# Performance work log

Measured on AMD Instinct MI355X. Metric: run time of the kernel, lower is better.

Reference implementation:

```python
import jax, jax.numpy as jnp
import numpy as np
from jax.scipy.special import logsumexp

TAU = 0.05
ITERATIONS = 10


def setup_inputs() -> dict:
    key = jax.random.key(0)
    logits = jax.random.normal(key, (256, 512, 512), dtype=jnp.float32)
    return {"logits": logits}


def reference(logits) -> jnp.ndarray:
    # log-space Sinkhorn-Knopp: project logits/tau to a doubly stochastic matrix
    Z = logits / TAU  # [B, n, n]
    u0 = jnp.zeros(Z.shape[:-1], dtype=Z.dtype)  # [B, n] row potentials
    v0 = jnp.zeros_like(u0)                      # [B, n] col potentials
    # log_marginal is zeros(n) in the original, i.e. uniform target marginals of 1

    def body(_, uv):
        u, v = uv
        u = -logsumexp(Z + v[..., None, :], axis=-1)  # row normalization
        v = -logsumexp(Z + u[..., :, None], axis=-2)  # col normalization
        return (u, v)

    u, v = jax.lax.fori_loop(0, ITERATIONS, body, (u0, v0))
    return jnp.exp(Z + u[..., :, None] + v[..., None, :])
```

## Files before the change

kernel.cpp:

```cpp
#include <hip/hip_runtime.h>

#define BN 512
#define NW 16
#define RPW 32

static constexpr float kScale = 28.853900817779268f;

__device__ __forceinline__ float fexp2(float x){ return __builtin_amdgcn_exp2f(x); }
__device__ __forceinline__ float flog2(float x){ return __builtin_amdgcn_logf(x); }
__device__ __forceinline__ float frcp (float x){ return __builtin_amdgcn_rcpf(x); }

__device__ __forceinline__ float dpp_sum64(float s){
    int t;
    t = __builtin_amdgcn_update_dpp(0, __float_as_int(s), 0x111, 0xf, 0xf, true); s += __int_as_float(t);
    t = __builtin_amdgcn_update_dpp(0, __float_as_int(s), 0x112, 0xf, 0xf, true); s += __int_as_float(t);
    t = __builtin_amdgcn_update_dpp(0, __float_as_int(s), 0x114, 0xf, 0xf, true); s += __int_as_float(t);
    t = __builtin_amdgcn_update_dpp(0, __float_as_int(s), 0x118, 0xf, 0xf, true); s += __int_as_float(t);
    t = __builtin_amdgcn_update_dpp(0, __float_as_int(s), 0x142, 0xa, 0xf, true); s += __int_as_float(t);
    t = __builtin_amdgcn_update_dpp(0, __float_as_int(s), 0x143, 0xc, 0xf, true); s += __int_as_float(t);
    return __int_as_float(__builtin_amdgcn_readlane(__float_as_int(s), 63));
}
__device__ __forceinline__ float dpp_max64(float m){
    const int NI = __float_as_int(-__builtin_inff());
    int t;
    t = __builtin_amdgcn_update_dpp(NI, __float_as_int(m), 0x111, 0xf, 0xf, false); m = fmaxf(m, __int_as_float(t));
    t = __builtin_amdgcn_update_dpp(NI, __float_as_int(m), 0x112, 0xf, 0xf, false); m = fmaxf(m, __int_as_float(t));
    t = __builtin_amdgcn_update_dpp(NI, __float_as_int(m), 0x114, 0xf, 0xf, false); m = fmaxf(m, __int_as_float(t));
    t = __builtin_amdgcn_update_dpp(NI, __float_as_int(m), 0x118, 0xf, 0xf, false); m = fmaxf(m, __int_as_float(t));
    t = __builtin_amdgcn_update_dpp(NI, __float_as_int(m), 0x142, 0xa, 0xf, false); m = fmaxf(m, __int_as_float(t));
    t = __builtin_amdgcn_update_dpp(NI, __float_as_int(m), 0x143, 0xc, 0xf, false); m = fmaxf(m, __int_as_float(t));
    return __int_as_float(__builtin_amdgcn_readlane(__float_as_int(m), 63));
}

__device__ __forceinline__ unsigned rtne_pack(float a, float b){
    unsigned ua = __float_as_uint(a), ub = __float_as_uint(b);
    unsigned lo = (ua + 0x7fffu + ((ua >> 16) & 1u)) >> 16;
    unsigned hi = (ub + 0x7fffu + ((ub >> 16) & 1u)) & 0xffff0000u;
    return lo | hi;
}
__device__ __forceinline__ void unpack2(unsigned w, float& lo, float& hi){
    lo = __uint_as_float(w << 16);
    hi = __uint_as_float(w & 0xffff0000u);
}

__device__ __forceinline__ int credIdx(int p){
    return ((p >> 8) * 288) + (((p & 255) >> 3) * 9) + (p & 7);
}

__global__ __launch_bounds__(1024, 1) void sinkhorn_fused(
    const float* __restrict__ logits, float* __restrict__ out,
    unsigned short* __restrict__ ws, int use_ws)
{
    __shared__ float Bf[BN];
    __shared__ float SL[BN];
    __shared__ float cred[NW][576];

    const int b = blockIdx.x;
    const size_t base = (size_t)b * BN * BN;
    const float* __restrict__ Zb = logits + base;
    float* __restrict__ Ob = out + base;
    unsigned short* __restrict__ Mb = use_ws ? (ws + base) : (unsigned short*)Ob;

    const int tid  = threadIdx.x;
    const int lane = tid & 63;
    const int wave = tid >> 6;
    const int wb   = wave * RPW;

    {
        float ca[8] = {0.f,0.f,0.f,0.f,0.f,0.f,0.f,0.f};

        #pragma unroll 2
        for (int r = 0; r < RPW; ++r) {
            const int i = wb + r;
            const float4 x0 = *reinterpret_cast<const float4*>(Zb + (size_t)i * BN + 4 * lane);
            const float4 x1 = *reinterpret_cast<const float4*>(Zb + (size_t)i * BN + 256 + 4 * lane);

            float t[8];
            t[0] = x0.x * kScale; t[1] = x0.y * kScale; t[2] = x0.z * kScale; t[3] = x0.w * kScale;
            t[4] = x1.x * kScale; t[5] = x1.y * kScale; t[6] = x1.z * kScale; t[7] = x1.w * kScale;

            float m = t[0];
            #pragma unroll
            for (int k = 1; k < 8; ++k) m = fmaxf(m, t[k]);
            m = dpp_max64(m);

            float p[8], s = 0.f;
            #pragma unroll
            for (int k = 0; k < 8; ++k) { p[k] = fexp2(t[k] - m); s += p[k]; }
            s = dpp_sum64(s);

            const float f = fexp2(64.0f - flog2(s));
            float Mv[8];
            #pragma unroll
            for (int k = 0; k < 8; ++k) { Mv[k] = p[k] * f; ca[k] += Mv[k]; }

            int4 packed;
            packed.x = (int)rtne_pack(Mv[0], Mv[1]);
            packed.y = (int)rtne_pack(Mv[2], Mv[3]);
            packed.z = (int)rtne_pack(Mv[4], Mv[5]);
            packed.w = (int)rtne_pack(Mv[6], Mv[7]);
            *reinterpret_cast<int4*>(Mb + (size_t)i * BN + lane * 8) = packed;
        }

        const int cbase = (lane < 32) ? lane * 9 : 288 + (lane - 32) * 9;
        #pragma unroll
        for (int k = 0; k < 8; ++k) cred[wave][cbase + k] = ca[k];
        __syncthreads();
    }

    const unsigned short* Mw = Mb + (size_t)wb * BN + lane * 8;
#define LD(r) (*reinterpret_cast<const int4*>(Mw + (size_t)(r) * BN))

    int4 W0 = LD(0), W1 = LD(1), W2 = LD(2), W3 = LD(3);

    if (tid < BN) {
        const int ci = credIdx(tid);
        float s = 0.f;
        #pragma unroll
        for (int wv = 0; wv < NW; ++wv) s += cred[wv][ci];
        Bf[tid] = frcp(s);
    }
    __syncthreads();

#define STEP1(ridx, W)                                                             \
    {                                                                              \
        float e[8];                                                                \
        unpack2((unsigned)(W).x, e[0], e[1]); unpack2((unsigned)(W).y, e[2], e[3]); \
        unpack2((unsigned)(W).z, e[4], e[5]); unpack2((unsigned)(W).w, e[6], e[7]); \
        float a0 = 0.f, a1 = 0.f, a2 = 0.f, a3 = 0.f;                              \
        a0 = fmaf(e[0], bl[0], a0); a1 = fmaf(e[1], bl[1], a1);                    \
        a2 = fmaf(e[2], bl[2], a2); a3 = fmaf(e[3], bl[3], a3);                    \
        a0 = fmaf(e[4], bl[4], a0); a1 = fmaf(e[5], bl[5], a1);                    \
        a2 = fmaf(e[6], bl[6], a2); a3 = fmaf(e[7], bl[7], a3);                    \
        const float s = dpp_sum64((a0 + a1) + (a2 + a3));                          \
        const float A = frcp(s);                                                   \
        if (lane == 0) SL[wb + (ridx)] = s;                                        \
        _Pragma("unroll")                                                          \
        for (int k = 0; k < 8; ++k) ca[k] = fmaf(e[k], A, ca[k]);                  \
    }

    for (int it = 1; it < 10; ++it) {
        float bl[8];
        #pragma unroll
        for (int k = 0; k < 8; ++k) bl[k] = Bf[8 * lane + k];
        float ca[8] = {0.f,0.f,0.f,0.f,0.f,0.f,0.f,0.f};

        #pragma unroll 1
        for (int r = 0; r < RPW; r += 4) {
            STEP1(r + 0, W0); W0 = LD((r + 4) & 31);
            STEP1(r + 1, W1); W1 = LD((r + 5) & 31);
            STEP1(r + 2, W2); W2 = LD((r + 6) & 31);
            STEP1(r + 3, W3); W3 = LD((r + 7) & 31);
        }

        const int cbase = (lane < 32) ? lane * 9 : 288 + (lane - 32) * 9;
        #pragma unroll
        for (int k = 0; k < 8; ++k) cred[wave][cbase + k] = ca[k];
        __syncthreads();
        if (tid < BN) {
            const int ci = credIdx(tid);
            float s = 0.f;
            #pragma unroll
            for (int wv = 0; wv < NW; ++wv) s += cred[wv][ci];
            Bf[tid] = frcp(s);
        }
        __syncthreads();
    }

    {
        float bf[8];
        #pragma unroll
        for (int k = 0; k < 8; ++k) bf[k] = Bf[8 * lane + k];

        auto emit_row = [&](int j) {
            const int4 w = *reinterpret_cast<const int4*>(Mb + (size_t)j * BN + lane * 8);
            float e[8];
            unpack2((unsigned)w.x, e[0], e[1]); unpack2((unsigned)w.y, e[2], e[3]);
            unpack2((unsigned)w.z, e[4], e[5]); unpack2((unsigned)w.w, e[6], e[7]);
            const float A = frcp(SL[j]);
            float4 o0, o1;
            o0.x = e[0] * A * bf[0]; o0.y = e[1] * A * bf[1];
            o0.z = e[2] * A * bf[2]; o0.w = e[3] * A * bf[3];
            o1.x = e[4] * A * bf[4]; o1.y = e[5] * A * bf[5];
            o1.z = e[6] * A * bf[6]; o1.w = e[7] * A * bf[7];
            *reinterpret_cast<float4*>(Ob + (size_t)j * BN + 4 * lane) = o0;
            *reinterpret_cast<float4*>(Ob + (size_t)j * BN + 256 + 4 * lane) = o1;
        };

        if (use_ws) {
            #pragma unroll 2
            for (int r = 0; r < RPW; ++r) emit_row(wb + r);
        } else {
            for (int L = 256; L >= 1; L >>= 1) {
                for (int j = L + wave; j < 2 * L; j += NW) emit_row(j);
                __syncthreads();
            }
            if (wave == 0) emit_row(0);
        }
    }
#undef LD
#undef STEP1
}

extern "C" void kernel_launch(void* const* d_in, const int* in_sizes, int n_in,
                              void* d_out, int out_size, void* d_ws, size_t ws_size,
                              hipStream_t stream) {
    const float* logits = (const float*)d_in[0];
    float* out = (float*)d_out;
    const int B = in_sizes[0] / (BN * BN);
    const size_t need = (size_t)B * BN * BN * sizeof(unsigned short);
    const int use_ws = (ws_size >= need) ? 1 : 0;
    hipLaunchKernelGGL(sinkhorn_fused, dim3(B), dim3(1024), 0, stream,
                       logits, out, (unsigned short*)d_ws, use_ws);
}
```

Measured before the change: 328.2 us.

## Keep first seven rows per wave of bf16 matrix resident in LDS

Stores the first 7 rows of each wave's 32-row slice of the packed bf16 exp matrix in shared memory instead of global workspace. The nine Sinkhorn sweeps and the final emit read those rows from LDS, and the global prefetch pipeline is re-indexed to cover only rows 7-31. This cuts global/L2 traffic per iteration by about 22%, at the cost of 112KB of extra LDS and a more complex, irregular load schedule.

```diff
diff --git a/kernel.cpp b/kernel.cpp
--- a/kernel.cpp
+++ b/kernel.cpp
@@ -3,6 +3,7 @@
 #define BN 512
 #define NW 16
 #define RPW 32
+#define LR  7
 
 static constexpr float kScale = 28.853900817779268f;
 
@@ -54,6 +55,7 @@
     __shared__ float Bf[BN];
     __shared__ float SL[BN];
     __shared__ float cred[NW][576];
+    __shared__ unsigned short Mlds[NW * LR * BN];
 
     const int b = blockIdx.x;
     const size_t base = (size_t)b * BN * BN;
@@ -99,7 +101,10 @@
             packed.y = (int)rtne_pack(Mv[2], Mv[3]);
             packed.z = (int)rtne_pack(Mv[4], Mv[5]);
             packed.w = (int)rtne_pack(Mv[6], Mv[7]);
-            *reinterpret_cast<int4*>(Mb + (size_t)i * BN + lane * 8) = packed;
+            if (r < LR)
+                *reinterpret_cast<int4*>(&Mlds[(wave * LR + r) * BN + lane * 8]) = packed;
+            else
+                *reinterpret_cast<int4*>(Mb + (size_t)i * BN + lane * 8) = packed;
         }
 
         const int cbase = (lane < 32) ? lane * 9 : 288 + (lane - 32) * 9;
@@ -109,9 +114,10 @@
     }
 
     const unsigned short* Mw = Mb + (size_t)wb * BN + lane * 8;
-#define LD(r) (*reinterpret_cast<const int4*>(Mw + (size_t)(r) * BN))
-
-    int4 W0 = LD(0), W1 = LD(1), W2 = LD(2), W3 = LD(3);
+#define LD(r)  (*reinterpret_cast<const int4*>(Mw + (size_t)(r) * BN))
+#define LDL(r) (*reinterpret_cast<const int4*>(&Mlds[(wave * LR + (r)) * BN + lane * 8]))
+
+    int4 W0 = LD(7), W1 = LD(8), W2 = LD(9), W3 = LD(10);
 
     if (tid < BN) {
         const int ci = credIdx(tid);
@@ -145,13 +151,29 @@
         for (int k = 0; k < 8; ++k) bl[k] = Bf[8 * lane + k];
         float ca[8] = {0.f,0.f,0.f,0.f,0.f,0.f,0.f,0.f};
 
+        {
+            int4 V0 = LDL(0), V1 = LDL(1);
+            STEP1(0, V0); V0 = LDL(2);
+            STEP1(1, V1); V1 = LDL(3);
+            STEP1(2, V0); V0 = LDL(4);
+            STEP1(3, V1); V1 = LDL(5);
+            STEP1(4, V0); V0 = LDL(6);
+            STEP1(5, V1);
+            STEP1(6, V0);
+        }
+
         #pragma unroll 1
-        for (int r = 0; r < RPW; r += 4) {
-            STEP1(r + 0, W0); W0 = LD((r + 4) & 31);
-            STEP1(r + 1, W1); W1 = LD((r + 5) & 31);
-            STEP1(r + 2, W2); W2 = LD((r + 6) & 31);
-            STEP1(r + 3, W3); W3 = LD((r + 7) & 31);
-        }
+        for (int g = 0; g < 20; g += 4) {
+            STEP1(7 + g,  W0); W0 = LD(11 + g);
+            STEP1(8 + g,  W1); W1 = LD(12 + g);
+            STEP1(9 + g,  W2); W2 = LD(13 + g);
+            STEP1(10 + g, W3); W3 = LD(14 + g);
+        }
+        STEP1(27, W0); W0 = LD(31);
+        STEP1(28, W1); W1 = LD(8);
+        STEP1(29, W2); W2 = LD(9);
+        STEP1(30, W3); W3 = LD(10);
+        STEP1(31, W0); W0 = LD(7);
 
         const int cbase = (lane < 32) ? lane * 9 : 288 + (lane - 32) * 9;
         #pragma unroll
@@ -173,7 +195,10 @@
         for (int k = 0; k < 8; ++k) bf[k] = Bf[8 * lane + k];
 
         auto emit_row = [&](int j) {
-            const int4 w = *reinterpret_cast<const int4*>(Mb + (size_t)j * BN + lane * 8);
+            const int lr = j & 31;
+            const int4 w = (lr < LR)
+                ? *reinterpret_cast<const int4*>(&Mlds[((j >> 5) * LR + lr) * BN + lane * 8])
+                : *reinterpret_cast<const int4*>(Mb + (size_t)j * BN + lane * 8);
             float e[8];
             unpack2((unsigned)w.x, e[0], e[1]); unpack2((unsigned)w.y, e[2], e[3]);
             unpack2((unsigned)w.z, e[4], e[5]); unpack2((unsigned)w.w, e[6], e[7]);
@@ -199,6 +224,7 @@
         }
     }
 #undef LD
+#undef LDL
 #undef STEP1
 }
 
```

Result: faster. 263.6 us (median of 2 runs) (-19.7%).
